# Optimization experiments

Measured on AMD Instinct MI355X. Metric: run time of the kernel, lower is better.

Reference implementation:

```python
import jax, jax.numpy as jnp
import numpy as np

BOUNDING_PERC = 0.05

def setup_inputs() -> dict:
    key = jax.random.key(0)
    ks = jax.random.split(key, 8)
    b, nfaces, ncells, nb, in_dim, ksz = 4, 1_000_000, 500_000, 500_000, 4, 9
    kernel = jax.random.normal(ks[0], (b, nfaces, in_dim), dtype=jnp.float32)
    source = jax.random.normal(ks[1], (b, nfaces, 3, 3), dtype=jnp.float32)
    ucenters = jax.random.normal(ks[2], (b, ncells), dtype=jnp.float32)
    W = jax.random.normal(ks[3], (in_dim, ksz), dtype=jnp.float32)
    bias = jax.random.normal(ks[4], (ksz,), dtype=jnp.float32)
    positions = jnp.arange(nb, dtype=jnp.int32)  # unique boundary-face ids
    owners = jax.random.randint(ks[5], (nb,), 0, ncells, dtype=jnp.int32)
    neighbours = jax.random.randint(ks[6], (nb,), 0, ncells, dtype=jnp.int32)
    return {"kernel": kernel, "source": source, "ucenters": ucenters,
            "W": W, "bias": bias, "positions": positions,
            "owners": owners, "neighbours": neighbours}

def reference(kernel, source, ucenters, W, bias, positions, owners, neighbours):
    # constraint layer: affine map to per-face stencil coefficients [b, nfaces, ksz]
    coefficients = jnp.einsum('bxi,is->bxs', kernel, W) + bias
    b, nfaces = source.shape[0], source.shape[1]
    patches = source.reshape(b, nfaces, -1)          # [b, nfaces, ksz]
    ufaces = jnp.einsum('bxs,bxs->bx', coefficients, patches)  # [b, nfaces]
    # --- bounding on boundary faces ---
    ufaces_b = ufaces[:, positions]                   # [b, nb]
    owner = ucenters[:, owners]                       # [b, nb]
    neighbour = ucenters[:, neighbours]               # [b, nb]
    side_max = jnp.maximum(owner, neighbour)
    side_min = jnp.minimum(owner, neighbour)
    flux_cd = 0.5 * (owner + neighbour)
    upwind = jnp.where(flux_cd >= 0.0, owner, neighbour)
    upper_lim = side_max + BOUNDING_PERC * jnp.abs(side_max)
    lower_lim = side_min - BOUNDING_PERC * jnp.abs(side_min)
    valid = (ufaces_b >= lower_lim) & (ufaces_b <= upper_lim)
    ufaces_bounded = jnp.where(valid, ufaces_b, upwind)
    # scatter bounded values back into the full face array
    return ufaces.at[:, positions].set(ufaces_bounded)
```

## Files before the change

### kernel.cpp

```cpp
#include <hip/hip_runtime.h>

#define BOUNDING_PERC 0.05f

__global__ __launch_bounds__(256) void scatter_inv_kernel(
    const int* __restrict__ pos, int* __restrict__ inv, int nb)
{
    int j = blockIdx.x * blockDim.x + threadIdx.x;
    if (j < nb) inv[pos[j]] = j;
}

__global__ __launch_bounds__(256) void fused_kernel(
    const float4* __restrict__ k4,
    const float4* __restrict__ s4,
    const float*  __restrict__ W,
    const float*  __restrict__ bias,
    const int*    __restrict__ inv,
    const float*  __restrict__ uc,
    const int*    __restrict__ own,
    const int*    __restrict__ nei,
    float*        __restrict__ out,
    int nfaces, int ncells)
{
    __shared__ float s_src[2304];
    const int tid   = threadIdx.x;
    const int gbase = blockIdx.x << 8;
    const int g     = gbase + tid;
    const int bb    = g / nfaces;
    const int f     = g - bb * nfaces;

    {
        const float4* src_blk = s4 + ((size_t)gbase * 9) / 4;
        float4* sm4 = reinterpret_cast<float4*>(s_src);
        sm4[tid]       = src_blk[tid];
        sm4[tid + 256] = src_blk[tid + 256];
        if (tid < 64) sm4[tid + 512] = src_blk[tid + 512];
    }

    float Wr[4][9];
#pragma unroll
    for (int i = 0; i < 4; ++i)
#pragma unroll
        for (int s = 0; s < 9; ++s)
            Wr[i][s] = W[i * 9 + s];
    float br[9];
#pragma unroll
    for (int s = 0; s < 9; ++s) br[s] = bias[s];

    const float4 kv = k4[g];
    const int j = inv[f];

    __syncthreads();

    const float* S = &s_src[tid * 9];
    float acc = 0.0f;
#pragma unroll
    for (int s = 0; s < 9; ++s) {
        float c = br[s];
        c = fmaf(kv.x, Wr[0][s], c);
        c = fmaf(kv.y, Wr[1][s], c);
        c = fmaf(kv.z, Wr[2][s], c);
        c = fmaf(kv.w, Wr[3][s], c);
        acc = fmaf(c, S[s], acc);
    }

    float res = acc;
    if (j >= 0) {
        float o = uc[bb * ncells + own[j]];
        float n = uc[bb * ncells + nei[j]];
        float smax = fmaxf(o, n);
        float smin = fminf(o, n);
        float flux = 0.5f * (o + n);
        float up   = (flux >= 0.0f) ? o : n;
        float hi   = smax + BOUNDING_PERC * fabsf(smax);
        float lo   = smin - BOUNDING_PERC * fabsf(smin);
        bool valid = (acc >= lo) && (acc <= hi);
        res = valid ? acc : up;
    }
    out[g] = res;
}

__global__ __launch_bounds__(256) void ufaces_kernel(
    const float4* __restrict__ k4, const float4* __restrict__ s4,
    const float* __restrict__ W, const float* __restrict__ bias,
    float* __restrict__ out)
{
    __shared__ float s_src[2304];
    const int tid = threadIdx.x;
    const int base_face = blockIdx.x << 8;
    {
        const float4* src_blk = s4 + ((size_t)base_face * 9) / 4;
        float4* sm4 = reinterpret_cast<float4*>(s_src);
        sm4[tid]       = src_blk[tid];
        sm4[tid + 256] = src_blk[tid + 256];
        if (tid < 64) sm4[tid + 512] = src_blk[tid + 512];
    }
    float Wr[4][9];
#pragma unroll
    for (int i = 0; i < 4; ++i)
#pragma unroll
        for (int s = 0; s < 9; ++s) Wr[i][s] = W[i * 9 + s];
    float br[9];
#pragma unroll
    for (int s = 0; s < 9; ++s) br[s] = bias[s];
    const float4 kv = k4[base_face + tid];
    __syncthreads();
    const float* S = &s_src[tid * 9];
    float acc = 0.0f;
#pragma unroll
    for (int s = 0; s < 9; ++s) {
        float c = br[s];
        c = fmaf(kv.x, Wr[0][s], c);
        c = fmaf(kv.y, Wr[1][s], c);
        c = fmaf(kv.z, Wr[2][s], c);
        c = fmaf(kv.w, Wr[3][s], c);
        acc = fmaf(c, S[s], acc);
    }
    out[base_face + tid] = acc;
}

__global__ __launch_bounds__(256) void bound_kernel(
    const float* __restrict__ uc, const int* __restrict__ pos,
    const int* __restrict__ own, const int* __restrict__ nei,
    float* __restrict__ out, int nb, int nfaces, int ncells, int nbatch)
{
    int idx = blockIdx.x * blockDim.x + threadIdx.x;
    if (idx >= nbatch * nb) return;
    int j  = idx % nb;
    int bb = idx / nb;
    int p = pos[j];
    float uf = out[bb * nfaces + p];
    float o  = uc[bb * ncells + own[j]];
    float n  = uc[bb * ncells + nei[j]];
    float smax = fmaxf(o, n);
    float smin = fminf(o, n);
    float flux = 0.5f * (o + n);
    float up   = (flux >= 0.0f) ? o : n;
    float hi   = smax + BOUNDING_PERC * fabsf(smax);
    float lo   = smin - BOUNDING_PERC * fabsf(smin);
    bool valid = (uf >= lo) && (uf <= hi);
    out[bb * nfaces + p] = valid ? uf : up;
}

extern "C" void kernel_launch(void* const* d_in, const int* in_sizes, int n_in,
                              void* d_out, int out_size, void* d_ws, size_t ws_size,
                              hipStream_t stream)
{
    const float* kernel_in  = (const float*)d_in[0];
    const float* source     = (const float*)d_in[1];
    const float* ucenters   = (const float*)d_in[2];
    const float* W          = (const float*)d_in[3];
    const float* bias       = (const float*)d_in[4];
    const int*   positions  = (const int*)d_in[5];
    const int*   owners     = (const int*)d_in[6];
    const int*   neighbours = (const int*)d_in[7];
    float*       out        = (float*)d_out;

    const int b      = 4;
    const int in_dim = 4;
    const int nfaces = in_sizes[0] / (b * in_dim);
    const int ncells = in_sizes[2] / b;
    const int nb     = in_sizes[5];
    const int total_faces = b * nfaces;

    if (ws_size >= (size_t)nfaces * sizeof(int)) {
        int* inv = (int*)d_ws;
        hipMemsetAsync(inv, 0xFF, (size_t)nfaces * sizeof(int), stream);
        scatter_inv_kernel<<<(nb + 255) / 256, 256, 0, stream>>>(positions, inv, nb);
        fused_kernel<<<total_faces / 256, 256, 0, stream>>>(
            (const float4*)kernel_in, (const float4*)source, W, bias,
            inv, ucenters, owners, neighbours, out, nfaces, ncells);
    } else {
        ufaces_kernel<<<total_faces / 256, 256, 0, stream>>>(
            (const float4*)kernel_in, (const float4*)source, W, bias, out);
        int total = b * nb;
        bound_kernel<<<(total + 255) / 256, 256, 0, stream>>>(
            ucenters, positions, owners, neighbours, out, nb, nfaces, ncells, b);
    }
}
```

Before: 61.94 us.

## Make fused kernel persistent with register prefetch of next tile

The fused kernel becomes a persistent grid-stride loop over 256-face tiles, launched with at most 2048 blocks. Each iteration loads the next tile's source and kernel data into registers before computing the current tile, so global loads overlap with compute and the boundary gathers. Shared-memory staging is now split into per-wave 64-lane slices, which removes the block-wide __syncthreads. This relies on in-order LDS access within a wavefront for correctness, and holding the prefetched tile raises register pressure.

```diff
diff --git a/kernel.cpp b/kernel.cpp
--- a/kernel.cpp
+++ b/kernel.cpp
@@ -19,22 +19,14 @@
     const int*    __restrict__ own,
     const int*    __restrict__ nei,
     float*        __restrict__ out,
-    int nfaces, int ncells)
-{
-    __shared__ float s_src[2304];
-    const int tid   = threadIdx.x;
-    const int gbase = blockIdx.x << 8;
-    const int g     = gbase + tid;
-    const int bb    = g / nfaces;
-    const int f     = g - bb * nfaces;
-
-    {
-        const float4* src_blk = s4 + ((size_t)gbase * 9) / 4;
-        float4* sm4 = reinterpret_cast<float4*>(s_src);
-        sm4[tid]       = src_blk[tid];
-        sm4[tid + 256] = src_blk[tid + 256];
-        if (tid < 64) sm4[tid + 512] = src_blk[tid + 512];
-    }
+    int nfaces, int ncells, int ntiles)
+{
+    __shared__ float4 sm[576];
+    const int tid  = threadIdx.x;
+    const int wv   = tid >> 6;
+    const int lane = tid & 63;
+    float4* mysm = sm + wv * 144;
+    const float* S = reinterpret_cast<const float*>(mysm) + lane * 9;
 
     float Wr[4][9];
 #pragma unroll
@@ -46,37 +38,70 @@
 #pragma unroll
     for (int s = 0; s < 9; ++s) br[s] = bias[s];
 
-    const float4 kv = k4[g];
-    const int j = inv[f];
-
-    __syncthreads();
-
-    const float* S = &s_src[tid * 9];
-    float acc = 0.0f;
-#pragma unroll
-    for (int s = 0; s < 9; ++s) {
-        float c = br[s];
-        c = fmaf(kv.x, Wr[0][s], c);
-        c = fmaf(kv.y, Wr[1][s], c);
-        c = fmaf(kv.z, Wr[2][s], c);
-        c = fmaf(kv.w, Wr[3][s], c);
-        acc = fmaf(c, S[s], acc);
-    }
-
-    float res = acc;
-    if (j >= 0) {
-        float o = uc[bb * ncells + own[j]];
-        float n = uc[bb * ncells + nei[j]];
-        float smax = fmaxf(o, n);
-        float smin = fminf(o, n);
-        float flux = 0.5f * (o + n);
-        float up   = (flux >= 0.0f) ? o : n;
-        float hi   = smax + BOUNDING_PERC * fabsf(smax);
-        float lo   = smin - BOUNDING_PERC * fabsf(smin);
-        bool valid = (acc >= lo) && (acc <= hi);
-        res = valid ? acc : up;
-    }
-    out[g] = res;
+    const int stride = gridDim.x;
+    int tile = blockIdx.x;
+    if (tile >= ntiles) return;
+
+    const float4* sb = s4 + (size_t)tile * 576 + wv * 144;
+    float4 a0 = sb[lane];
+    float4 a1 = sb[lane + 64];
+    float4 a2;
+    if (lane < 16) a2 = sb[lane + 128];
+    float4 kv = k4[(size_t)tile * 256 + tid];
+
+    while (true) {
+        const int nt = tile + stride;
+        float4 b0, b1, b2, kv2;
+        if (nt < ntiles) {
+            const float4* sb2 = s4 + (size_t)nt * 576 + wv * 144;
+            b0 = sb2[lane];
+            b1 = sb2[lane + 64];
+            if (lane < 16) b2 = sb2[lane + 128];
+            kv2 = k4[(size_t)nt * 256 + tid];
+        }
+
+        mysm[lane]      = a0;
+        mysm[lane + 64] = a1;
+        if (lane < 16) mysm[lane + 128] = a2;
+
+        const int gbase = tile << 8;
+        const int g     = gbase + tid;
+        const int ubb   = gbase / nfaces;
+        int f  = gbase - ubb * nfaces + tid;
+        int bb = ubb;
+        if (f >= nfaces) { f -= nfaces; ++bb; }
+        const int j = inv[f];
+
+        float acc = 0.0f;
+#pragma unroll
+        for (int s = 0; s < 9; ++s) {
+            float c = br[s];
+            c = fmaf(kv.x, Wr[0][s], c);
+            c = fmaf(kv.y, Wr[1][s], c);
+            c = fmaf(kv.z, Wr[2][s], c);
+            c = fmaf(kv.w, Wr[3][s], c);
+            acc = fmaf(c, S[s], acc);
+        }
+
+        float res = acc;
+        if (j >= 0) {
+            float o = uc[bb * ncells + own[j]];
+            float n = uc[bb * ncells + nei[j]];
+            float smax = fmaxf(o, n);
+            float smin = fminf(o, n);
+            float flux = 0.5f * (o + n);
+            float up   = (flux >= 0.0f) ? o : n;
+            float hi   = smax + BOUNDING_PERC * fabsf(smax);
+            float lo   = smin - BOUNDING_PERC * fabsf(smin);
+            bool valid = (acc >= lo) && (acc <= hi);
+            res = valid ? acc : up;
+        }
+        out[g] = res;
+
+        if (nt >= ntiles) break;
+        a0 = b0; a1 = b1; a2 = b2; kv = kv2;
+        tile = nt;
+    }
 }
 
 __global__ __launch_bounds__(256) void ufaces_kernel(
@@ -161,14 +186,18 @@
     const int ncells = in_sizes[2] / b;
     const int nb     = in_sizes[5];
     const int total_faces = b * nfaces;
+    const int ntiles = total_faces / 256;
 
     if (ws_size >= (size_t)nfaces * sizeof(int)) {
         int* inv = (int*)d_ws;
         hipMemsetAsync(inv, 0xFF, (size_t)nfaces * sizeof(int), stream);
         scatter_inv_kernel<<<(nb + 255) / 256, 256, 0, stream>>>(positions, inv, nb);
-        fused_kernel<<<total_faces / 256, 256, 0, stream>>>(
+
+        int grid = 2048;
+        if (grid > ntiles) grid = ntiles;
+        fused_kernel<<<grid, 256, 0, stream>>>(
             (const float4*)kernel_in, (const float4*)source, W, bias,
-            inv, ucenters, owners, neighbours, out, nfaces, ncells);
+            inv, ucenters, owners, neighbours, out, nfaces, ncells, ntiles);
     } else {
         ufaces_kernel<<<total_faces / 256, 256, 0, stream>>>(
             (const float4*)kernel_in, (const float4*)source, W, bias, out);
```

Result: slower. 79.21 us (+27.9%).

## Pre-scatter owner/neighbour ids per face and use per-wave shared staging

Applied to the files above, without the earlier changes.

The inverse-index table is replaced by two face-indexed tables holding owner and neighbour cell ids directly, which removes one level of dependent gather in the fused kernel. Each wavefront now stages only its own slice of the source patches in shared memory, so the block-wide barrier is dropped. The ucenters gathers are also issued before the stencil math so their latency can overlap with it. In exchange the prep kernel writes twice as much workspace, and the fused kernel reads an extra face-indexed int array.

```diff
diff --git a/kernel.cpp b/kernel.cpp
--- a/kernel.cpp
+++ b/kernel.cpp
@@ -2,11 +2,17 @@
 
 #define BOUNDING_PERC 0.05f
 
-__global__ __launch_bounds__(256) void scatter_inv_kernel(
-    const int* __restrict__ pos, int* __restrict__ inv, int nb)
+__global__ __launch_bounds__(256) void scatter_on_kernel(
+    const int* __restrict__ pos, const int* __restrict__ own,
+    const int* __restrict__ nei,
+    int* __restrict__ own_f, int* __restrict__ nei_f, int nb)
 {
     int j = blockIdx.x * blockDim.x + threadIdx.x;
-    if (j < nb) inv[pos[j]] = j;
+    if (j < nb) {
+        int p = pos[j];
+        own_f[p] = own[j];
+        nei_f[p] = nei[j];
+    }
 }
 
 __global__ __launch_bounds__(256) void fused_kernel(
@@ -14,26 +20,45 @@
     const float4* __restrict__ s4,
     const float*  __restrict__ W,
     const float*  __restrict__ bias,
-    const int*    __restrict__ inv,
+    const int*    __restrict__ own_f,
+    const int*    __restrict__ nei_f,
     const float*  __restrict__ uc,
-    const int*    __restrict__ own,
-    const int*    __restrict__ nei,
     float*        __restrict__ out,
     int nfaces, int ncells)
 {
-    __shared__ float s_src[2304];
-    const int tid   = threadIdx.x;
+    __shared__ float smem[2304];
+    const int tid  = threadIdx.x;
+    const int wv   = tid >> 6;
+    const int lane = tid & 63;
+    float* mysm = smem + wv * 576;
+
     const int gbase = blockIdx.x << 8;
-    const int g     = gbase + tid;
-    const int bb    = g / nfaces;
-    const int f     = g - bb * nfaces;
+    const int gw    = gbase + (wv << 6);
+    const int g     = gw + lane;
 
-    {
-        const float4* src_blk = s4 + ((size_t)gbase * 9) / 4;
-        float4* sm4 = reinterpret_cast<float4*>(s_src);
-        sm4[tid]       = src_blk[tid];
-        sm4[tid + 256] = src_blk[tid + 256];
-        if (tid < 64) sm4[tid + 512] = src_blk[tid + 512];
+    const float4* sb  = s4 + ((size_t)gw * 9) / 4;
+    const float*  sbf = reinterpret_cast<const float*>(sb);
+    float4 a0 = sb[lane];
+    float4 a1 = sb[lane + 64];
+    float  a2 = sbf[512 + lane];
+    float4 kv = k4[g];
+
+    const int bb = g / nfaces;
+    const int f  = g - bb * nfaces;
+    const int ow = own_f[f];
+    const int nw = nei_f[f];
+
+    float4* mysm4 = reinterpret_cast<float4*>(mysm);
+    mysm4[lane]      = a0;
+    mysm4[lane + 64] = a1;
+    mysm[512 + lane] = a2;
+
+    float o = 0.0f, n = 0.0f;
+    const bool lim = (ow >= 0);
+    if (lim) {
+        const float* ucb = uc + (size_t)bb * ncells;
+        o = ucb[ow];
+        n = ucb[nw];
     }
 
     float Wr[4][9];
@@ -46,12 +71,7 @@
 #pragma unroll
     for (int s = 0; s < 9; ++s) br[s] = bias[s];
 
-    const float4 kv = k4[g];
-    const int j = inv[f];
-
-    __syncthreads();
-
-    const float* S = &s_src[tid * 9];
+    const float* S = mysm + lane * 9;
     float acc = 0.0f;
 #pragma unroll
     for (int s = 0; s < 9; ++s) {
@@ -64,9 +84,7 @@
     }
 
     float res = acc;
-    if (j >= 0) {
-        float o = uc[bb * ncells + own[j]];
-        float n = uc[bb * ncells + nei[j]];
+    if (lim) {
         float smax = fmaxf(o, n);
         float smin = fminf(o, n);
         float flux = 0.5f * (o + n);
@@ -162,13 +180,15 @@
     const int nb     = in_sizes[5];
     const int total_faces = b * nfaces;
 
-    if (ws_size >= (size_t)nfaces * sizeof(int)) {
-        int* inv = (int*)d_ws;
-        hipMemsetAsync(inv, 0xFF, (size_t)nfaces * sizeof(int), stream);
-        scatter_inv_kernel<<<(nb + 255) / 256, 256, 0, stream>>>(positions, inv, nb);
+    if (ws_size >= 2 * (size_t)nfaces * sizeof(int)) {
+        int* own_f = (int*)d_ws;
+        int* nei_f = own_f + nfaces;
+        hipMemsetAsync(own_f, 0xFF, (size_t)nfaces * sizeof(int), stream);
+        scatter_on_kernel<<<(nb + 255) / 256, 256, 0, stream>>>(
+            positions, owners, neighbours, own_f, nei_f, nb);
         fused_kernel<<<total_faces / 256, 256, 0, stream>>>(
             (const float4*)kernel_in, (const float4*)source, W, bias,
-            inv, ucenters, owners, neighbours, out, nfaces, ncells);
+            own_f, nei_f, ucenters, out, nfaces, ncells);
     } else {
         ufaces_kernel<<<total_faces / 256, 256, 0, stream>>>(
             (const float4*)kernel_in, (const float4*)source, W, bias, out);
```

After: 61.30 us. About the same (-1.0%).
